# Kernel tuning notes

Measured on AMD Instinct MI355X. Metric: run time of the kernel, lower is better.

## Reference

```python
import jax, jax.numpy as jnp
import numpy as np

ITER_ROUTING = 3
EPS = 1e-9


def squash(s):
    # s: [C, H]; standard capsule squash along last dim
    norm_sq = jnp.sum(s * s, axis=-1, keepdims=True)
    return s * (norm_sq / (1.0 + norm_sq)) / jnp.sqrt(norm_sq + EPS)


def setup_inputs() -> dict:
    key = jax.random.key(0)
    k1, k2 = jax.random.split(key)
    C, K, H = 512, 64, 1024
    encoder_output = jax.random.normal(k1, (C, K, H), dtype=jnp.float32)
    # nn.Linear(H, H, bias=False) weight, scaled like kaiming-uniform-ish init
    W = jax.random.normal(k2, (H, H), dtype=jnp.float32) * (1.0 / np.sqrt(H))
    return {"encoder_output": encoder_output, "W": W}


def reference(encoder_output, W):
    C, K, H = encoder_output.shape
    # Linear projection (loop-invariant: l_1 is fixed, so hoist out of routing loop)
    # torch Linear computes x @ W.T
    hat = jnp.einsum('ckh,oh->cko', encoder_output, W)  # [C, K, H]
    b = jnp.zeros((C, K), dtype=encoder_output.dtype)
    c = None
    for _ in range(ITER_ROUTING):
        d = jax.nn.softmax(b, axis=-1)                  # [C, K]
        c_hat = jnp.einsum('ckh,ck->ch', hat, d)        # [C, H] weighted sum
        c = squash(c_hat)                               # [C, H]
        b = b + jnp.einsum('ckh,ch->ck', hat, c)        # agreement update
    return c
```

## Files before the change

### kernel.cpp

```cpp
#include <hip/hip_runtime.h>
#include <hip/hip_bf16.h>
#include <cstdint>


#define C_DIM 512
#define KCAPS 64
#define H_DIM 1024
#define M_DIM (C_DIM * KCAPS)

typedef _Float16 h8 __attribute__((ext_vector_type(8)));
typedef _Float16 h4 __attribute__((ext_vector_type(4)));
typedef float f4 __attribute__((ext_vector_type(4)));

__global__ void cvt_f32_f16(const float* __restrict__ in, _Float16* __restrict__ out, int n4) {
    int i = blockIdx.x * blockDim.x + threadIdx.x;
    int stride = gridDim.x * blockDim.x;
    for (; i < n4; i += stride) {
        float4 v = ((const float4*)in)[i];
        h4 o;
        o[0] = (_Float16)v.x; o[1] = (_Float16)v.y;
        o[2] = (_Float16)v.z; o[3] = (_Float16)v.w;
        ((h4*)out)[i] = o;
    }
}

__device__ __forceinline__ void gload16(const _Float16* g, _Float16* l) {
    __builtin_amdgcn_global_load_lds(
        (const __attribute__((address_space(1))) void*)g,
        (__attribute__((address_space(3))) void*)l, 16, 0, 0);
}

__global__ __launch_bounds__(256) void gemm_f16_bt(const _Float16* __restrict__ A,
                                                   const _Float16* __restrict__ B,
                                                   _Float16* __restrict__ Cmat) {
    __shared__ _Float16 As[128 * 64] __attribute__((aligned(16)));
    __shared__ _Float16 Bs[128 * 64] __attribute__((aligned(16)));
    const int tid  = threadIdx.x;
    const int lane = tid & 63;
    const int wid  = tid >> 6;
    const int tm   = blockIdx.x >> 3;
    const int tn   = blockIdx.x & 7;
    const int wr   = wid >> 1, wc = wid & 1;

    f4 acc[4][4] = {};

    const int r8 = lane >> 3;
    const int c8 = (lane & 7) * 8;

    const _Float16* Abase = A + (size_t)(tm * 128) * H_DIM;
    const _Float16* Bbase = B + (size_t)(tn * 128) * H_DIM;

    for (int kt = 0; kt < H_DIM; kt += 64) {
        #pragma unroll
        for (int i = 0; i < 4; ++i) {
            const int chunk = wid * 4 + i;
            const int row   = chunk * 8 + r8;
            gload16(Abase + (size_t)row * H_DIM + kt + c8, &As[chunk * 512]);
            gload16(Bbase + (size_t)row * H_DIM + kt + c8, &Bs[chunk * 512]);
        }
        __syncthreads();

        #pragma unroll
        for (int kk = 0; kk < 64; kk += 32) {
            h8 af[4], bf[4];
            const int kidx = kk + ((lane >> 4) << 3);
            #pragma unroll
            for (int m = 0; m < 4; ++m)
                af[m] = *(const h8*)&As[(wr * 64 + m * 16 + (lane & 15)) * 64 + kidx];
            #pragma unroll
            for (int n = 0; n < 4; ++n)
                bf[n] = *(const h8*)&Bs[(wc * 64 + n * 16 + (lane & 15)) * 64 + kidx];
            #pragma unroll
            for (int m = 0; m < 4; ++m)
                #pragma unroll
                for (int n = 0; n < 4; ++n)
                    acc[m][n] = __builtin_amdgcn_mfma_f32_16x16x32_f16(af[m], bf[n], acc[m][n], 0, 0, 0);
        }
        __syncthreads();
    }

    const int crow0 = tm * 128 + wr * 64;
    const int ccol0 = tn * 128 + wc * 64;
    #pragma unroll
    for (int m = 0; m < 4; ++m) {
        #pragma unroll
        for (int n = 0; n < 4; ++n) {
            const int col = ccol0 + n * 16 + (lane & 15);
            #pragma unroll
            for (int q = 0; q < 4; ++q) {
                const int row = crow0 + m * 16 + (lane >> 4) * 4 + q;
                Cmat[(size_t)row * H_DIM + col] = (_Float16)acc[m][n][q];
            }
        }
    }
}

__device__ __forceinline__ float2 upk(unsigned int u) {
    unsigned short ul = (unsigned short)(u & 0xffffu);
    unsigned short uh = (unsigned short)(u >> 16);
    _Float16 lo, hi;
    __builtin_memcpy(&lo, &ul, 2);
    __builtin_memcpy(&hi, &uh, 2);
    return make_float2((float)lo, (float)hi);
}

__global__ __launch_bounds__(512) void routing_kernel(const _Float16* __restrict__ hat,
                                                      float* __restrict__ out) {
    const int c    = blockIdx.x;
    const int t    = threadIdx.x;
    const int lane = t & 63;
    const int wid  = t >> 6;

    __shared__ float b_lds[64];
    __shared__ float d_lds[64];
    __shared__ float red[8];
    __shared__ float bpart[8][64];
    __shared__ float norm_sh;

    unsigned int hp[64];
    const unsigned int* base = (const unsigned int*)(hat + (size_t)c * KCAPS * H_DIM) + t;
    #pragma unroll
    for (int k = 0; k < 64; ++k) hp[k] = base[k * (H_DIM / 2)];

    if (t < 64) b_lds[t] = 0.0f;
    __syncthreads();

    float cx = 0.0f, cy = 0.0f;

    for (int it = 0; it < 3; ++it) {
        if (t < 64) {
            float bv = b_lds[t];
            float mx = bv;
            #pragma unroll
            for (int s = 1; s < 64; s <<= 1) mx = fmaxf(mx, __shfl_xor(mx, s, 64));
            float e = __expf(bv - mx);
            float sum = e;
            #pragma unroll
            for (int s = 1; s < 64; s <<= 1) sum += __shfl_xor(sum, s, 64);
            d_lds[t] = e / sum;
        }
        __syncthreads();

        float chx = 0.0f, chy = 0.0f;
        #pragma unroll
        for (int k = 0; k < 64; ++k) {
            float2 f = upk(hp[k]);
            float dk = d_lds[k];
            chx = fmaf(f.x, dk, chx);
            chy = fmaf(f.y, dk, chy);
        }

        float nn = chx * chx + chy * chy;
        #pragma unroll
        for (int s = 1; s < 64; s <<= 1) nn += __shfl_xor(nn, s, 64);
        if (lane == 0) red[wid] = nn;
        __syncthreads();
        if (t == 0) {
            float tot = 0.0f;
            #pragma unroll
            for (int w = 0; w < 8; ++w) tot += red[w];
            norm_sh = tot;
        }
        __syncthreads();
        const float ns = norm_sh;
        const float scale = (ns / (1.0f + ns)) / sqrtf(ns + 1e-9f);
        cx = chx * scale;
        cy = chy * scale;

        if (it < 2) {
            float v[32];
            #pragma unroll
            for (int i = 0; i < 32; ++i) {
                float2 fa = upk(hp[2 * i]);
                float2 fb = upk(hp[2 * i + 1]);
                float pa = fmaf(fa.x, cx, fa.y * cy);
                float pb = fmaf(fb.x, cx, fb.y * cy);
                const bool hi = (lane & 1) != 0;
                float keep = hi ? pb : pa;
                float send = hi ? pa : pb;
                v[i] = keep + __shfl_xor(send, 1, 64);
            }
            #pragma unroll
            for (int bit = 1; bit < 6; ++bit) {
                const int s = 1 << bit;
                const int n = 64 >> (bit + 1);
                const bool hi = (lane & s) != 0;
                #pragma unroll
                for (int i = 0; i < n; ++i) {
                    float keep = hi ? v[2 * i + 1] : v[2 * i];
                    float send = hi ? v[2 * i] : v[2 * i + 1];
                    v[i] = keep + __shfl_xor(send, s, 64);
                }
            }
            bpart[wid][lane] = v[0];
            __syncthreads();
            if (t < 64) {
                float s = 0.0f;
                #pragma unroll
                for (int w = 0; w < 8; ++w) s += bpart[w][t];
                b_lds[t] += s;
            }
            __syncthreads();
        }
    }

    float2 o;
    o.x = cx; o.y = cy;
    *(float2*)&out[(size_t)c * H_DIM + 2 * t] = o;
}

extern "C" void kernel_launch(void* const* d_in, const int* in_sizes, int n_in,
                              void* d_out, int out_size, void* d_ws, size_t ws_size,
                              hipStream_t stream) {
    const float* enc = (const float*)d_in[0];
    const float* Wf  = (const float*)d_in[1];
    float* out = (float*)d_out;

    char* ws = (char*)d_ws;
    _Float16* enc16 = (_Float16*)ws;
    _Float16* W16   = (_Float16*)(ws + (size_t)67108864);
    _Float16* hat16 = (_Float16*)(ws + (size_t)67108864 + 2097152);

    const int n_enc = C_DIM * KCAPS * H_DIM;
    const int n_w   = H_DIM * H_DIM;

    cvt_f32_f16<<<2048, 256, 0, stream>>>(enc, enc16, n_enc / 4);
    cvt_f32_f16<<<512, 256, 0, stream>>>(Wf, W16, n_w / 4);

    gemm_f16_bt<<<(M_DIM / 128) * (H_DIM / 128), 256, 0, stream>>>(enc16, W16, hat16);

    routing_kernel<<<C_DIM, 512, 0, stream>>>(hat16, out);
}
```

Baseline: 332.6 us.

## Stage routing hat tile in LDS and swizzle GEMM block order

```diff
diff --git a/kernel.cpp b/kernel.cpp
--- a/kernel.cpp
+++ b/kernel.cpp
@@ -38,8 +38,10 @@
     const int tid  = threadIdx.x;
     const int lane = tid & 63;
     const int wid  = tid >> 6;
-    const int tm   = blockIdx.x >> 3;
-    const int tn   = blockIdx.x & 7;
+    const int bid  = blockIdx.x;
+    const int swz  = (bid & 7) * 256 + (bid >> 3);
+    const int tm   = swz >> 3;
+    const int tn   = swz & 7;
     const int wr   = wid >> 1, wc = wid & 1;
 
     f4 acc[4][4] = {};
@@ -104,32 +106,34 @@
     return make_float2((float)lo, (float)hi);
 }
 
-__global__ __launch_bounds__(512) void routing_kernel(const _Float16* __restrict__ hat,
-                                                      float* __restrict__ out) {
+__global__ __launch_bounds__(512) void routing2(const _Float16* __restrict__ hat,
+                                                float* __restrict__ out) {
+    __shared__ _Float16 hat_s[KCAPS * H_DIM] __attribute__((aligned(16)));
+    __shared__ float b_lds[KCAPS];
+    __shared__ float d_lds[KCAPS];
+    __shared__ float c_lds[H_DIM];
+    __shared__ float red[8];
+    __shared__ float norm_sh;
+
     const int c    = blockIdx.x;
     const int t    = threadIdx.x;
     const int lane = t & 63;
     const int wid  = t >> 6;
 
-    __shared__ float b_lds[64];
-    __shared__ float d_lds[64];
-    __shared__ float red[8];
-    __shared__ float bpart[8][64];
-    __shared__ float norm_sh;
-
-    unsigned int hp[64];
-    const unsigned int* base = (const unsigned int*)(hat + (size_t)c * KCAPS * H_DIM) + t;
+    const _Float16* gbase = hat + (size_t)c * (KCAPS * H_DIM);
     #pragma unroll
-    for (int k = 0; k < 64; ++k) hp[k] = base[k * (H_DIM / 2)];
-
+    for (int i = 0; i < 16; ++i) {
+        const int chunk = wid * 16 + i;
+        gload16(gbase + chunk * 512 + lane * 8, &hat_s[chunk * 512]);
+    }
     if (t < 64) b_lds[t] = 0.0f;
     __syncthreads();
 
     float cx = 0.0f, cy = 0.0f;
 
     for (int it = 0; it < 3; ++it) {
-        if (t < 64) {
-            float bv = b_lds[t];
+        if (wid == 0) {
+            float bv = b_lds[lane];
             float mx = bv;
             #pragma unroll
             for (int s = 1; s < 64; s <<= 1) mx = fmaxf(mx, __shfl_xor(mx, s, 64));
@@ -137,14 +141,15 @@
             float sum = e;
             #pragma unroll
             for (int s = 1; s < 64; s <<= 1) sum += __shfl_xor(sum, s, 64);
-            d_lds[t] = e / sum;
+            d_lds[lane] = e / sum;
         }
         __syncthreads();
 
         float chx = 0.0f, chy = 0.0f;
         #pragma unroll
         for (int k = 0; k < 64; ++k) {
-            float2 f = upk(hp[k]);
+            unsigned int u = *(const unsigned int*)&hat_s[k * H_DIM + 2 * t];
+            float2 f = upk(u);
             float dk = d_lds[k];
             chx = fmaf(f.x, dk, chx);
             chy = fmaf(f.y, dk, chy);
@@ -167,41 +172,35 @@
         cx = chx * scale;
         cy = chy * scale;
 
-        if (it < 2) {
-            float v[32];
-            #pragma unroll
-            for (int i = 0; i < 32; ++i) {
-                float2 fa = upk(hp[2 * i]);
-                float2 fb = upk(hp[2 * i + 1]);
-                float pa = fmaf(fa.x, cx, fa.y * cy);
-                float pb = fmaf(fb.x, cx, fb.y * cy);
-                const bool hi = (lane & 1) != 0;
-                float keep = hi ? pb : pa;
-                float send = hi ? pa : pb;
-                v[i] = keep + __shfl_xor(send, 1, 64);
+        if (it == 2) break;
+
+        c_lds[2 * t]     = cx;
+        c_lds[2 * t + 1] = cy;
+        __syncthreads();
+
+        float4 cc[4];
+        #pragma unroll
+        for (int q = 0; q < 4; ++q)
+            cc[q] = *(const float4*)&c_lds[lane * 16 + q * 4];
+
+        #pragma unroll
+        for (int j = 0; j < 8; ++j) {
+            const int k = wid * 8 + j;
+            const h8* hp = (const h8*)&hat_s[k * H_DIM + lane * 16];
+            float p = 0.0f;
+            #pragma unroll
+            for (int half = 0; half < 2; ++half) {
+                h8 v = hp[half];
+                const float* cf = (const float*)&cc[half * 2];
+                #pragma unroll
+                for (int e = 0; e < 8; ++e)
+                    p = fmaf((float)v[e], cf[e], p);
             }
             #pragma unroll
-            for (int bit = 1; bit < 6; ++bit) {
-                const int s = 1 << bit;
-                const int n = 64 >> (bit + 1);
-                const bool hi = (lane & s) != 0;
-                #pragma unroll
-                for (int i = 0; i < n; ++i) {
-                    float keep = hi ? v[2 * i + 1] : v[2 * i];
-                    float send = hi ? v[2 * i] : v[2 * i + 1];
-                    v[i] = keep + __shfl_xor(send, s, 64);
-                }
-            }
-            bpart[wid][lane] = v[0];
-            __syncthreads();
-            if (t < 64) {
-                float s = 0.0f;
-                #pragma unroll
-                for (int w = 0; w < 8; ++w) s += bpart[w][t];
-                b_lds[t] += s;
-            }
-            __syncthreads();
-        }
+            for (int s = 1; s < 64; s <<= 1) p += __shfl_xor(p, s, 64);
+            if (lane == 0) b_lds[k] += p;
+        }
+        __syncthreads();
     }
 
     float2 o;
@@ -229,5 +228,5 @@
 
     gemm_f16_bt<<<(M_DIM / 128) * (H_DIM / 128), 256, 0, stream>>>(enc16, W16, hat16);
 
-    routing_kernel<<<C_DIM, 512, 0, stream>>>(hat16, out);
-}
+    routing2<<<C_DIM, 512, 0, stream>>>(hat16, out);
+}
```

Result: no change. 336.9 us (+1.3%).
